# Performance work log

Hardware: AMD Instinct MI355X
Metric: run time of the kernel (lower is better)

The kernel has to match this reference:

```python
import jax, jax.numpy as jnp
import numpy as np
from jax import lax

STRIDE = 4
PAD = 3
TOP_K = 2
LOSS_COEF = 1e-2
LN_EPS = 1e-6


def _expert(x, W, b, ln_w, ln_b):
    # Conv2d(c1->c2, k=7, stride=4, pad=3) + channel-first LayerNorm (over C only)
    y = lax.conv_general_dilated(x, W, (STRIDE, STRIDE), [(PAD, PAD), (PAD, PAD)],
                                 dimension_numbers=("NCHW", "OIHW", "NCHW"))
    y = y + b[None, :, None, None]
    u = y.mean(1, keepdims=True)
    s = ((y - u) ** 2).mean(1, keepdims=True)
    y = (y - u) / jnp.sqrt(s + LN_EPS)
    return ln_w[None, :, None, None] * y + ln_b[None, :, None, None]


def _cv_squared(v):
    v = v.astype(jnp.float32)
    return jnp.var(v, ddof=1) / (jnp.mean(v) ** 2 + 1e-10)


def setup_inputs() -> dict:
    key = jax.random.key(0)
    ks = jax.random.split(key, 10)
    B, C1, H, W = 32, 3, 224, 224
    C2, E, KS = 64, 8, 7
    return {
        "x": jax.random.normal(ks[0], (B, C1, H, W), jnp.float32),
        "expert_W": jax.random.normal(ks[1], (E, C2, C1, KS, KS), jnp.float32) * 0.05,
        "expert_b": jax.random.normal(ks[2], (E, C2), jnp.float32) * 0.02,
        "expert_ln_w": jnp.ones((E, C2), jnp.float32),
        "expert_ln_b": jnp.zeros((E, C2), jnp.float32),
        "shared_W": jax.random.normal(ks[3], (C2, C1, KS, KS), jnp.float32) * 0.05,
        "shared_b": jax.random.normal(ks[4], (C2,), jnp.float32) * 0.02,
        "shared_ln_w": jnp.ones((C2,), jnp.float32),
        "shared_ln_b": jnp.zeros((C2,), jnp.float32),
        "w_gate": jax.random.normal(ks[5], (C1, E), jnp.float32) * 0.1,
    }


def reference(x, expert_W, expert_b, expert_ln_w, expert_ln_b,
              shared_W, shared_b, shared_ln_w, shared_ln_b, w_gate):
    B = x.shape[0]
    E = w_gate.shape[1]
    # --- noisy_top_k_gating (eval path: clean logits, no noise) ---
    gate_inp = x.mean(axis=(2, 3))                     # [B, width=c1]
    logits = gate_inp @ w_gate                          # [B, E]
    top_vals, top_idx = lax.top_k(logits, TOP_K)        # [B, k]
    top_gates = jax.nn.softmax(top_vals, axis=1)        # [B, k]
    gates = jnp.zeros((B, E), logits.dtype).at[jnp.arange(B)[:, None], top_idx].set(top_gates)
    # --- load-balancing aux loss ---
    importance = gates.sum(0)
    load = (gates > 0).sum(0).astype(jnp.float32)
    loss = LOSS_COEF * (_cv_squared(importance) + _cv_squared(load))
    # --- dispatch/combine: dense-equivalent of SparseDispatcher ---
    # output[b] = sum_e gates[b,e] * expert_e(x[b])  (zero gates mask out experts)
    expert_outs = jax.vmap(lambda W, b, lw, lb: _expert(x, W, b, lw, lb))(
        expert_W, expert_b, expert_ln_w, expert_ln_b)   # [E, B, C2, H', W']
    y = jnp.einsum("be,ebchw->bchw", gates, expert_outs)
    y = y + _expert(x, shared_W, shared_b, shared_ln_w, shared_ln_b)
    return y, loss
```

## Files before the change

kernel.cpp:

```cpp
#include <hip/hip_runtime.h>
#include <cstdint>
#include <cstddef>

static constexpr int BATCH = 32;
static constexpr int CIN   = 3;
static constexpr int HIN   = 224, WIN = 224;
static constexpr int COUT  = 64;
static constexpr int HOUT  = 56, WOUT = 56;
static constexpr int NPIX  = HOUT * WOUT;
static constexpr int NEXP  = 8;
static constexpr int KROWS = 21;
static constexpr int NKS   = 6;
static constexpr int NGRP  = 28;
static constexpr int PWL   = 232;
static constexpr int WR    = 11;
static constexpr float LN_EPS_F = 1e-6f;

static constexpr int PW3_ELEMS = 9 * 4 * 6 * 64 * 8;

static constexpr int N_GPART  = BATCH * CIN * 8;
static constexpr int N_REPACK = (PW3_ELEMS + 255) / 256;

typedef __bf16 bf16x8 __attribute__((ext_vector_type(8)));
typedef float  f32x4  __attribute__((ext_vector_type(4)));

__device__ __align__(16) ushort g_pw3[PW3_ELEMS];
__device__ float g_gatepart[BATCH * CIN * 8];

__device__ __forceinline__ ushort f2bf(float f) {
  uint u = __float_as_uint(f);
  uint r = (u + 0x7FFFu + ((u >> 16) & 1u)) >> 16;
  return (ushort)r;
}

__global__ __launch_bounds__(256) void k_pre(const float* __restrict__ x,
                                             const float* __restrict__ eW,
                                             const float* __restrict__ sW) {
  const int bid = blockIdx.x;
  if (bid < N_GPART) {
    const int plane = bid >> 3;
    const int slice = bid & 7;
    const float4* p4 = reinterpret_cast<const float4*>(x + (size_t)plane * (HIN * WIN));
    float s = 0.f;
    const int i0 = slice * 1568;
    for (int i = i0 + (int)threadIdx.x; i < i0 + 1568; i += 256) {
      const float4 v = p4[i];
      s += v.x + v.y + v.z + v.w;
    }
    __shared__ float red[256];
    red[threadIdx.x] = s;
    __syncthreads();
    for (int off = 128; off > 0; off >>= 1) {
      if ((int)threadIdx.x < off) red[threadIdx.x] += red[threadIdx.x + off];
      __syncthreads();
    }
    if (threadIdx.x == 0) g_gatepart[bid] = red[0];
  } else {
    const int idx = (bid - N_GPART) * 256 + threadIdx.x;
    if (idx >= PW3_ELEMS) return;
    const int j    = idx & 7;
    const int lane = (idx >> 3) & 63;
    const int ks   = (idx >> 9) % 6;
    const int fe   = idx / (512 * 6);
    const int f    = fe & 3;
    const int e    = fe >> 2;
    const int m    = lane >> 4;
    const int colA = lane & 15;
    const int co   = f * 16 + colA;
    const int r    = ks * 4 + m;
    float v = 0.f;
    if (j >= 1 && r < KROWS) {
      const int k = r * 7 + (j - 1);
      v = (e < 8) ? eW[(size_t)(e * COUT + co) * 147 + k]
                  : sW[(size_t)co * 147 + k];
    }
    g_pw3[idx] = f2bf(v);
  }
}

__global__ __launch_bounds__(448, 3) void k_main(
    const float* __restrict__ x,
    const float* __restrict__ w_gate,
    const float* __restrict__ eB, const float* __restrict__ sB,
    const float* __restrict__ elnw, const float* __restrict__ elnb,
    const float* __restrict__ slnw, const float* __restrict__ slnb,
    float* __restrict__ out, float* __restrict__ loss_out) {
  __shared__ __align__(16) ushort Wnd[3 * WR * PWL];

  const int tid  = threadIdx.x;
  const int lane = tid & 63;
  const int w    = tid >> 6;
  const int b    = blockIdx.x / NGRP;
  const int G    = blockIdx.x % NGRP;

  for (int i = tid; i < 3 * WR * 28; i += 448) {
    const int j8 = i % 28;
    const int rr = i / 28;
    const int ci = rr / WR;
    const int wr = rr - ci * WR;
    const int ih = 8 * G + wr - 3;
    uint2 lo = {0u, 0u}, hi = {0u, 0u};
    if ((unsigned)ih < (unsigned)HIN) {
      const float4* xr = reinterpret_cast<const float4*>(
          x + ((size_t)(b * CIN + ci) * HIN + ih) * WIN);
      const float4 f0 = xr[2 * j8];
      const float4 f1 = xr[2 * j8 + 1];
      lo.x = (uint)f2bf(f0.x) | ((uint)f2bf(f0.y) << 16);
      lo.y = (uint)f2bf(f0.z) | ((uint)f2bf(f0.w) << 16);
      hi.x = (uint)f2bf(f1.x) | ((uint)f2bf(f1.y) << 16);
      hi.y = (uint)f2bf(f1.z) | ((uint)f2bf(f1.w) << 16);
    }
    *reinterpret_cast<uint2*>(&Wnd[rr * PWL + 8 * j8 + 4]) = lo;
    *reinterpret_cast<uint2*>(&Wnd[rr * PWL + 8 * j8 + 8]) = hi;
    if (j8 == 0)  { const uint2 z = {0u, 0u}; *reinterpret_cast<uint2*>(&Wnd[rr * PWL]) = z; }
    if (j8 == 27) { const uint2 z = {0u, 0u}; *reinterpret_cast<uint2*>(&Wnd[rr * PWL + 228]) = z; }
  }

  float gi[3];
  #pragma unroll
  for (int c = 0; c < 3; ++c) {
    float s = 0.f;
    #pragma unroll
    for (int p = 0; p < 8; ++p) s += g_gatepart[(b * 3 + c) * 8 + p];
    gi[c] = s * (1.f / (float)(HIN * WIN));
  }
  float best1 = -1e30f, best2 = -1e30f;
  int i1 = 0, i2 = 0;
  #pragma unroll
  for (int e = 0; e < NEXP; ++e) {
    const float lg = gi[0] * w_gate[e] + gi[1] * w_gate[8 + e] + gi[2] * w_gate[16 + e];
    if (lg > best1) { best2 = best1; i2 = i1; best1 = lg; i1 = e; }
    else if (lg > best2) { best2 = lg; i2 = e; }
  }
  const float e21 = expf(best2 - best1);
  const float g1 = 1.f / (1.f + e21);
  const float g2 = e21 / (1.f + e21);
  const int e1 = __builtin_amdgcn_readfirstlane(i1);
  const int e2 = __builtin_amdgcn_readfirstlane(i2);

  if (blockIdx.x == 0 && w == 0) {
    float mg1 = 0.f, mg2 = 0.f;
    int me1 = -1, me2 = -1;
    if (lane < BATCH) {
      float a[3];
      #pragma unroll
      for (int c = 0; c < 3; ++c) {
        float s = 0.f;
        #pragma unroll
        for (int p = 0; p < 8; ++p) s += g_gatepart[(lane * 3 + c) * 8 + p];
        a[c] = s * (1.f / (float)(HIN * WIN));
      }
      float b1 = -1e30f, b2 = -1e30f;
      int j1 = 0, j2 = 0;
      #pragma unroll
      for (int e = 0; e < NEXP; ++e) {
        const float lg = a[0] * w_gate[e] + a[1] * w_gate[8 + e] + a[2] * w_gate[16 + e];
        if (lg > b1) { b2 = b1; j2 = j1; b1 = lg; j1 = e; }
        else if (lg > b2) { b2 = lg; j2 = e; }
      }
      const float q = expf(b2 - b1);
      mg1 = 1.f / (1.f + q); mg2 = q / (1.f + q);
      me1 = j1; me2 = j2;
    }
    float imp[NEXP], lod[NEXP];
    #pragma unroll
    for (int e = 0; e < NEXP; ++e) {
      float ie = ((me1 == e) ? mg1 : 0.f) + ((me2 == e) ? mg2 : 0.f);
      float le = (((me1 == e) && (mg1 > 0.f)) ? 1.f : 0.f)
               + (((me2 == e) && (mg2 > 0.f)) ? 1.f : 0.f);
      #pragma unroll
      for (int o = 32; o > 0; o >>= 1) { ie += __shfl_xor(ie, o, 64); le += __shfl_xor(le, o, 64); }
      imp[e] = ie; lod[e] = le;
    }
    if (lane == 0) {
      float mi = 0.f, ml = 0.f;
      #pragma unroll
      for (int e = 0; e < NEXP; ++e) { mi += imp[e]; ml += lod[e]; }
      mi *= (1.f / NEXP); ml *= (1.f / NEXP);
      float vi = 0.f, vl = 0.f;
      #pragma unroll
      for (int e = 0; e < NEXP; ++e) {
        const float di = imp[e] - mi; vi += di * di;
        const float dl = lod[e] - ml; vl += dl * dl;
      }
      vi *= (1.f / (NEXP - 1)); vl *= (1.f / (NEXP - 1));
      loss_out[0] = 0.01f * (vi / (mi * mi + 1e-10f) + vl / (ml * ml + 1e-10f));
    }
  }

  const int m    = lane >> 4;
  const int colA = lane & 15;
  const int eidx[3] = {e1, e2, 8};
  const float ge[3] = {g1, g2, 1.f};

  int Crow[NKS];
  #pragma unroll
  for (int ks = 0; ks < NKS; ++ks) {
    int r = 4 * ks + m;
    r = r > 20 ? 20 : r;
    const int ci = r >= 14 ? 2 : (r >= 7 ? 1 : 0);
    const int kh = r - ci * 7;
    Crow[ks] = (ci * WR + kh) * PWL;
  }

  const int pg = G * 112 + w * 16 + colA;
  const int oh = pg / WOUT;
  const int ow = pg - oh * WOUT;
  const int baseB = ((oh - 2 * G) * 4) * PWL + ow * 4;

  __syncthreads();

  float outAcc[16];
  #pragma unroll
  for (int j = 0; j < 16; ++j) outAcc[j] = 0.f;

  #pragma unroll
  for (int e = 0; e < 3; ++e) {
    const int es = eidx[e];
    f32x4 acc[4];
    #pragma unroll
    for (int f = 0; f < 4; ++f) acc[f] = (f32x4){0.f, 0.f, 0.f, 0.f};

    const ushort* ape = g_pw3 + (size_t)es * (4 * 6 * 512) + lane * 8;
    #pragma unroll
    for (int ks = 0; ks < NKS; ++ks) {
      bf16x8 a4[4];
      #pragma unroll
      for (int f = 0; f < 4; ++f)
        a4[f] = __builtin_bit_cast(bf16x8, *reinterpret_cast<const uint4*>(
            ape + (f * 6 + ks) * 512));
      const ushort* p = &Wnd[baseB + Crow[ks]];
      const uint2 lo = *reinterpret_cast<const uint2*>(p);
      const uint2 hi = *reinterpret_cast<const uint2*>(p + 4);
      const uint4 raw = {lo.x, lo.y, hi.x, hi.y};
      const bf16x8 bf = __builtin_bit_cast(bf16x8, raw);
      #pragma unroll
      for (int f = 0; f < 4; ++f)
        acc[f] = __builtin_amdgcn_mfma_f32_16x16x32_bf16(a4[f], bf, acc[f], 0, 0, 0);
    }

    const float* bsrc = (e < 2) ? eB + es * COUT : sB;
    const float* wsrc = (e < 2) ? elnw + es * COUT : slnw;
    const float* csrc = (e < 2) ? elnb + es * COUT : slnb;
    float s = 0.f, q = 0.f;
    #pragma unroll
    for (int f = 0; f < 4; ++f) {
      const float4 b4 = *reinterpret_cast<const float4*>(bsrc + f * 16 + m * 4);
      #pragma unroll
      for (int r = 0; r < 4; ++r) {
        const float y = acc[f][r] + (&b4.x)[r];
        acc[f][r] = y;
        s += y; q += y * y;
      }
    }
    s += __shfl_xor(s, 16, 64); s += __shfl_xor(s, 32, 64);
    q += __shfl_xor(q, 16, 64); q += __shfl_xor(q, 32, 64);
    const float u  = s * (1.f / 64.f);
    const float vv = q * (1.f / 64.f) - u * u;
    const float rs = rsqrtf(vv + LN_EPS_F);
    #pragma unroll
    for (int f = 0; f < 4; ++f) {
      const float4 lw4 = *reinterpret_cast<const float4*>(wsrc + f * 16 + m * 4);
      const float4 lb4 = *reinterpret_cast<const float4*>(csrc + f * 16 + m * 4);
      #pragma unroll
      for (int r = 0; r < 4; ++r)
        outAcc[f * 4 + r] += ge[e] * ((&lw4.x)[r] * (acc[f][r] - u) * rs + (&lb4.x)[r]);
    }
  }

  float* const outb = out + (size_t)b * (COUT * NPIX);
  #pragma unroll
  for (int f = 0; f < 4; ++f)
    #pragma unroll
    for (int r = 0; r < 4; ++r)
      outb[(size_t)(f * 16 + m * 4 + r) * NPIX + pg] = outAcc[f * 4 + r];
}

extern "C" void kernel_launch(void* const* d_in, const int* in_sizes, int n_in,
                              void* d_out, int out_size, void* d_ws, size_t ws_size,
                              hipStream_t stream) {
  const float* x    = (const float*)d_in[0];
  const float* eW   = (const float*)d_in[1];
  const float* eB   = (const float*)d_in[2];
  const float* elnw = (const float*)d_in[3];
  const float* elnb = (const float*)d_in[4];
  const float* sW   = (const float*)d_in[5];
  const float* sB   = (const float*)d_in[6];
  const float* slnw = (const float*)d_in[7];
  const float* slnb = (const float*)d_in[8];
  const float* wg   = (const float*)d_in[9];
  float* out = (float*)d_out;

  float* loss_ptr = out + (size_t)BATCH * COUT * NPIX;

  k_pre<<<N_GPART + N_REPACK, 256, 0, stream>>>(x, eW, sW);
  k_main<<<BATCH * NGRP, 448, 0, stream>>>(x, wg, eB, sB, elnw, elnb,
                                           slnw, slnb, out, loss_ptr);
}
```

Baseline: 47.09 us.

## Drop LDS input staging; load conv patches directly from global into registers

Removes the shared-memory staging of bf16 input rows and the block barrier. Each single-wave block now covers one 16-pixel tile and reads the needed input float4s straight from global memory, converting them to bf16 fragments held in registers. This cuts the LDS fill and the synchronisation, but it issues many more small blocks and re-reads overlapping input rows from global memory or cache instead of sharing them through LDS. Gate and top-k computation is now repeated in every one of the many small blocks.

Result: slower. 50.12 us (+6.4%).

```diff
diff --git a/kernel.cpp b/kernel.cpp
--- a/kernel.cpp
+++ b/kernel.cpp
@@ -11,9 +11,7 @@
 static constexpr int NEXP  = 8;
 static constexpr int KROWS = 21;
 static constexpr int NKS   = 6;
-static constexpr int NGRP  = 28;
-static constexpr int PWL   = 232;
-static constexpr int WR    = 11;
+static constexpr int NTILE = NPIX / 16;
 static constexpr float LN_EPS_F = 1e-6f;
 
 static constexpr int PW3_ELEMS = 9 * 4 * 6 * 64 * 8;
@@ -78,43 +76,18 @@
   }
 }
 
-__global__ __launch_bounds__(448, 3) void k_main(
+__global__ __launch_bounds__(64, 3) void k_main(
     const float* __restrict__ x,
     const float* __restrict__ w_gate,
     const float* __restrict__ eB, const float* __restrict__ sB,
     const float* __restrict__ elnw, const float* __restrict__ elnb,
     const float* __restrict__ slnw, const float* __restrict__ slnb,
     float* __restrict__ out, float* __restrict__ loss_out) {
-  __shared__ __align__(16) ushort Wnd[3 * WR * PWL];
-
-  const int tid  = threadIdx.x;
-  const int lane = tid & 63;
-  const int w    = tid >> 6;
-  const int b    = blockIdx.x / NGRP;
-  const int G    = blockIdx.x % NGRP;
-
-  for (int i = tid; i < 3 * WR * 28; i += 448) {
-    const int j8 = i % 28;
-    const int rr = i / 28;
-    const int ci = rr / WR;
-    const int wr = rr - ci * WR;
-    const int ih = 8 * G + wr - 3;
-    uint2 lo = {0u, 0u}, hi = {0u, 0u};
-    if ((unsigned)ih < (unsigned)HIN) {
-      const float4* xr = reinterpret_cast<const float4*>(
-          x + ((size_t)(b * CIN + ci) * HIN + ih) * WIN);
-      const float4 f0 = xr[2 * j8];
-      const float4 f1 = xr[2 * j8 + 1];
-      lo.x = (uint)f2bf(f0.x) | ((uint)f2bf(f0.y) << 16);
-      lo.y = (uint)f2bf(f0.z) | ((uint)f2bf(f0.w) << 16);
-      hi.x = (uint)f2bf(f1.x) | ((uint)f2bf(f1.y) << 16);
-      hi.y = (uint)f2bf(f1.z) | ((uint)f2bf(f1.w) << 16);
-    }
-    *reinterpret_cast<uint2*>(&Wnd[rr * PWL + 8 * j8 + 4]) = lo;
-    *reinterpret_cast<uint2*>(&Wnd[rr * PWL + 8 * j8 + 8]) = hi;
-    if (j8 == 0)  { const uint2 z = {0u, 0u}; *reinterpret_cast<uint2*>(&Wnd[rr * PWL]) = z; }
-    if (j8 == 27) { const uint2 z = {0u, 0u}; *reinterpret_cast<uint2*>(&Wnd[rr * PWL + 228]) = z; }
-  }
+  const int lane = threadIdx.x;
+  const int b    = blockIdx.x / NTILE;
+  const int tile = blockIdx.x % NTILE;
+  const int m    = lane >> 4;
+  const int colA = lane & 15;
 
   float gi[3];
   #pragma unroll
@@ -138,7 +111,7 @@
   const int e1 = __builtin_amdgcn_readfirstlane(i1);
   const int e2 = __builtin_amdgcn_readfirstlane(i2);
 
-  if (blockIdx.x == 0 && w == 0) {
+  if (blockIdx.x == 0) {
     float mg1 = 0.f, mg2 = 0.f;
     int me1 = -1, me2 = -1;
     if (lane < BATCH) {
@@ -188,27 +161,35 @@
     }
   }
 
-  const int m    = lane >> 4;
-  const int colA = lane & 15;
-  const int eidx[3] = {e1, e2, 8};
-  const float ge[3] = {g1, g2, 1.f};
-
-  int Crow[NKS];
+  const int pg = tile * 16 + colA;
+  const int oh = pg / WOUT;
+  const int ow = pg - oh * WOUT;
+  bf16x8 bfr[NKS];
   #pragma unroll
   for (int ks = 0; ks < NKS; ++ks) {
     int r = 4 * ks + m;
     r = r > 20 ? 20 : r;
     const int ci = r >= 14 ? 2 : (r >= 7 ? 1 : 0);
     const int kh = r - ci * 7;
-    Crow[ks] = (ci * WR + kh) * PWL;
-  }
-
-  const int pg = G * 112 + w * 16 + colA;
-  const int oh = pg / WOUT;
-  const int ow = pg - oh * WOUT;
-  const int baseB = ((oh - 2 * G) * 4) * PWL + ow * 4;
-
-  __syncthreads();
+    const int ih = oh * 4 + kh - 3;
+    float4 f0 = {0.f, 0.f, 0.f, 0.f};
+    float4 f1 = {0.f, 0.f, 0.f, 0.f};
+    if ((unsigned)ih < (unsigned)HIN) {
+      const float4* row4 = reinterpret_cast<const float4*>(
+          x + ((size_t)(b * CIN + ci) * HIN + ih) * WIN);
+      f1 = row4[ow];
+      if (ow > 0) f0 = row4[ow - 1];
+    }
+    const uint p0 = (uint)f2bf(f0.x) | ((uint)f2bf(f0.y) << 16);
+    const uint p1 = (uint)f2bf(f0.z) | ((uint)f2bf(f0.w) << 16);
+    const uint p2 = (uint)f2bf(f1.x) | ((uint)f2bf(f1.y) << 16);
+    const uint p3 = (uint)f2bf(f1.z) | ((uint)f2bf(f1.w) << 16);
+    const uint4 raw = {p0, p1, p2, p3};
+    bfr[ks] = __builtin_bit_cast(bf16x8, raw);
+  }
+
+  const int eidx[3] = {e1, e2, 8};
+  const float ge[3] = {g1, g2, 1.f};
 
   float outAcc[16];
   #pragma unroll
@@ -229,14 +210,9 @@
       for (int f = 0; f < 4; ++f)
         a4[f] = __builtin_bit_cast(bf16x8, *reinterpret_cast<const uint4*>(
             ape + (f * 6 + ks) * 512));
-      const ushort* p = &Wnd[baseB + Crow[ks]];
-      const uint2 lo = *reinterpret_cast<const uint2*>(p);
-      const uint2 hi = *reinterpret_cast<const uint2*>(p + 4);
-      const uint4 raw = {lo.x, lo.y, hi.x, hi.y};
-      const bf16x8 bf = __builtin_bit_cast(bf16x8, raw);
       #pragma unroll
       for (int f = 0; f < 4; ++f)
-        acc[f] = __builtin_amdgcn_mfma_f32_16x16x32_bf16(a4[f], bf, acc[f], 0, 0, 0);
+        acc[f] = __builtin_amdgcn_mfma_f32_16x16x32_bf16(a4[f], bfr[ks], acc[f], 0, 0, 0);
     }
 
     const float* bsrc = (e < 2) ? eB + es * COUT : sB;
@@ -294,6 +270,6 @@
   float* loss_ptr = out + (size_t)BATCH * COUT * NPIX;
 
   k_pre<<<N_GPART + N_REPACK, 256, 0, stream>>>(x, eW, sW);
-  k_main<<<BATCH * NGRP, 448, 0, stream>>>(x, wg, eB, sB, elnw, elnb,
+  k_main<<<BATCH * NTILE, 64, 0, stream>>>(x, wg, eB, sB, elnw, elnb,
                                            slnw, slnb, out, loss_ptr);
 }
```
